# Performance work log

Hardware: AMD Instinct MI355X
Metric: run time of the kernel (lower is better)

Reference implementation:

```python
import jax, jax.numpy as jnp
import numpy as np

NUM_LEVELS = 6
LEVEL_DIM = 4
BASE_RES = 4
HASHMAP_SIZE = 2 ** 19  # torch-ngp default log2_hashmap_size=19
N_SAMPLES = 300
PRIMES = (1, 2654435761, 805459861)
N_RAYS = 16384

# offsets of the 8 trilinear corners, [8,3]
_OFFS = jnp.array([[i, j, k] for i in (0, 1) for j in (0, 1) for k in (0, 1)], dtype=jnp.int32)


def _sample_points_along_ray(starts, ends):
    # starts/ends: [N,2]; lerp 300 points, append ray parameter t as z -> [N,300,3]
    t = jnp.linspace(0.0, 1.0, N_SAMPLES, dtype=starts.dtype)[None, :, None]  # [1,300,1]
    p2 = starts[:, None, :] * (1.0 - t) + ends[:, None, :] * t  # [N,300,2]
    z = jnp.broadcast_to(t, (starts.shape[0], N_SAMPLES, 1))
    return jnp.concatenate([p2, z], axis=-1)


def _grid_encode(points, embeddings):
    # points: [N,S,3] in [0,1]; embeddings: [L, T, D]. Returns [N,S,L*D].
    feats = []
    for l in range(NUM_LEVELS):
        R = BASE_RES * (2 ** l)  # 4,8,16,32,64,128
        pos = points * R
        p0 = jnp.floor(pos).astype(jnp.int32)
        w = pos - p0  # trilinear fractions, [N,S,3]
        corners = jnp.clip(p0[..., None, :] + _OFFS, 0, R)  # [N,S,8,3]
        cw = jnp.where(_OFFS.astype(bool), w[..., None, :], 1.0 - w[..., None, :]).prod(-1)  # [N,S,8]
        if (R + 1) ** 3 <= HASHMAP_SIZE:
            # dense level: row-major vertex index
            idx = corners[..., 0] + corners[..., 1] * (R + 1) + corners[..., 2] * (R + 1) ** 2
        else:
            # hashed level: xor of coord * prime, uint32 wraparound
            c = corners.astype(jnp.uint32)
            idx = ((c[..., 0] * jnp.uint32(PRIMES[0]))
                   ^ (c[..., 1] * jnp.uint32(PRIMES[1]))
                   ^ (c[..., 2] * jnp.uint32(PRIMES[2]))) % jnp.uint32(HASHMAP_SIZE)
            idx = idx.astype(jnp.int32)
        emb = embeddings[l][idx]  # [N,S,8,D] gather
        feats.append((cw[..., None] * emb).sum(-2))  # [N,S,D]
    return jnp.concatenate(feats, axis=-1)  # [N,S,24]


def setup_inputs() -> dict:
    key = jax.random.key(0)
    ks = jax.random.split(key, 12)
    x = jax.random.uniform(ks[0], (N_RAYS, 4), dtype=jnp.float32)
    indices_first = jax.random.randint(ks[1], (N_RAYS,), 0, N_SAMPLES, dtype=jnp.int32)
    # hash-grid tables, torch-ngp init: uniform(-1e-4, 1e-4)
    embeddings = jax.random.uniform(ks[2], (NUM_LEVELS, HASHMAP_SIZE, LEVEL_DIM),
                                    minval=-1e-4, maxval=1e-4, dtype=jnp.float32)
    d_in = NUM_LEVELS * LEVEL_DIM * 5  # 120
    sc = 0.02
    W1 = jax.random.normal(ks[3], (64, d_in), dtype=jnp.float32) * sc
    b1 = jnp.zeros((64,), jnp.float32)
    W2 = jax.random.normal(ks[4], (64, 64), dtype=jnp.float32) * sc
    b2 = jnp.zeros((64,), jnp.float32)
    W3 = jax.random.normal(ks[5], (64, 64), dtype=jnp.float32) * sc
    b3 = jnp.zeros((64,), jnp.float32)
    W4 = jax.random.normal(ks[6], (3, 64), dtype=jnp.float32) * sc
    b4 = jnp.zeros((3,), jnp.float32)
    return {"x": x, "indices_first": indices_first, "embeddings": embeddings,
            "W1": W1, "b1": b1, "W2": W2, "b2": b2, "W3": W3, "b3": b3, "W4": W4, "b4": b4}


def reference(x, indices_first, embeddings, W1, b1, W2, b2, W3, b3, W4, b4):
    pts = jax.lax.stop_gradient(_sample_points_along_ray(x[:, :2], x[:, 2:4]))  # no_grad in original
    pe = _grid_encode(pts, embeddings)  # [N,300,24]
    n = jnp.arange(x.shape[0])
    gather = lambda d: pe[n, jnp.clip(indices_first + d, 0, N_SAMPLES - 1)]
    feat = jnp.concatenate([gather(-2), gather(-1), gather(0), gather(1), gather(2)], axis=-1)  # [N,120]
    h = jax.nn.relu(feat @ W1.T + b1)
    h = jax.nn.relu(h @ W2.T + b2)
    h = jax.nn.relu(h @ W3.T + b3)
    return h @ W4.T + b4  # [N,3]
```

## Files before the change

### kernel.cpp

```cpp
#include <hip/hip_runtime.h>


#define NSAMP 300
#define HSIZE (1u << 19)

__global__ __launch_bounds__(1024, 1) void rgbnet_fused(
    const float4* __restrict__ x,
    const int*    __restrict__ idxf,
    const float4* __restrict__ emb,
    const float* __restrict__ W1, const float* __restrict__ b1,
    const float* __restrict__ W2, const float* __restrict__ b2,
    const float* __restrict__ W3, const float* __restrict__ b3,
    const float* __restrict__ W4, const float* __restrict__ b4,
    float* __restrict__ out, int N)
{
    __shared__ float sFeat[120 * 64];
    __shared__ float sHa[64 * 64];
    __shared__ float sHb[64 * 64];

    const int tid  = threadIdx.x;
    const int r    = tid & 63;
    const int wsub = tid >> 6;
    const int ray  = blockIdx.x * 64 + r;

    {
        const float4 xr = x[ray];
        const int    i0 = idxf[ray];
        const float sx = xr.x, sy = xr.y, ex = xr.z, ey = xr.w;

        for (int p = wsub; p < 30; p += 16) {
            const int d = p / 6;
            const int l = p - d * 6;
            int s = i0 + d - 2;
            s = max(0, min(s, NSAMP - 1));
            const float t   = (float)s * (1.0f / 299.0f);
            const float omt = 1.0f - t;
            const int   R   = 4 << l;
            const float fR  = (float)R;
            const float px = (sx * omt + ex * t) * fR;
            const float py = (sy * omt + ey * t) * fR;
            const float pz = t * fR;
            const float fx0 = floorf(px), fy0 = floorf(py), fz0 = floorf(pz);
            const float wx = px - fx0, wy = py - fy0, wz = pz - fz0;
            const int ix = (int)fx0, iy = (int)fy0, iz = (int)fz0;
            const int Rp1 = R + 1;
            const float4* __restrict__ ebase = emb + (size_t)l * HSIZE;

            float ax = 0.f, ay = 0.f, az = 0.f, aw = 0.f;
            #pragma unroll
            for (int c = 0; c < 8; ++c) {
                const int ox = (c >> 2) & 1, oy = (c >> 1) & 1, oz = c & 1;
                int cx = min(ix + ox, R); cx = max(cx, 0);
                int cy = min(iy + oy, R); cy = max(cy, 0);
                int cz = min(iz + oz, R); cz = max(cz, 0);
                unsigned idx;
                if (l < 5) {
                    idx = (unsigned)(cx + cy * Rp1 + cz * Rp1 * Rp1);
                } else {
                    idx = ((unsigned)cx * 1u
                         ^ (unsigned)cy * 2654435761u
                         ^ (unsigned)cz * 805459861u) & (HSIZE - 1u);
                }
                const float4 e = ebase[idx];
                const float cw = (ox ? wx : 1.f - wx)
                               * (oy ? wy : 1.f - wy)
                               * (oz ? wz : 1.f - wz);
                ax = fmaf(cw, e.x, ax);
                ay = fmaf(cw, e.y, ay);
                az = fmaf(cw, e.z, az);
                aw = fmaf(cw, e.w, aw);
            }
            const int k0 = p * 4;
            sFeat[(k0 + 0) * 64 + r] = ax;
            sFeat[(k0 + 1) * 64 + r] = ay;
            sFeat[(k0 + 2) * 64 + r] = az;
            sFeat[(k0 + 3) * 64 + r] = aw;
        }
    }
    __syncthreads();

    const int wu = __builtin_amdgcn_readfirstlane(wsub);
    const int j0 = wu * 4;

    float hh[4];

    #pragma unroll
    for (int jj = 0; jj < 4; ++jj) hh[jj] = b1[j0 + jj];
    #pragma unroll 2
    for (int kc = 0; kc < 120; kc += 4) {
        const float f0 = sFeat[(kc + 0) * 64 + r];
        const float f1 = sFeat[(kc + 1) * 64 + r];
        const float f2 = sFeat[(kc + 2) * 64 + r];
        const float f3 = sFeat[(kc + 3) * 64 + r];
        #pragma unroll
        for (int jj = 0; jj < 4; ++jj) {
            const float4 wv = *(const float4*)&W1[(j0 + jj) * 120 + kc];
            hh[jj] = fmaf(f0, wv.x, hh[jj]);
            hh[jj] = fmaf(f1, wv.y, hh[jj]);
            hh[jj] = fmaf(f2, wv.z, hh[jj]);
            hh[jj] = fmaf(f3, wv.w, hh[jj]);
        }
    }
    #pragma unroll
    for (int jj = 0; jj < 4; ++jj)
        sHa[(j0 + jj) * 64 + r] = fmaxf(hh[jj], 0.f);
    __syncthreads();

    #pragma unroll
    for (int jj = 0; jj < 4; ++jj) hh[jj] = b2[j0 + jj];
    #pragma unroll 2
    for (int kc = 0; kc < 64; kc += 4) {
        const float f0 = sHa[(kc + 0) * 64 + r];
        const float f1 = sHa[(kc + 1) * 64 + r];
        const float f2 = sHa[(kc + 2) * 64 + r];
        const float f3 = sHa[(kc + 3) * 64 + r];
        #pragma unroll
        for (int jj = 0; jj < 4; ++jj) {
            const float4 wv = *(const float4*)&W2[(j0 + jj) * 64 + kc];
            hh[jj] = fmaf(f0, wv.x, hh[jj]);
            hh[jj] = fmaf(f1, wv.y, hh[jj]);
            hh[jj] = fmaf(f2, wv.z, hh[jj]);
            hh[jj] = fmaf(f3, wv.w, hh[jj]);
        }
    }
    #pragma unroll
    for (int jj = 0; jj < 4; ++jj)
        sHb[(j0 + jj) * 64 + r] = fmaxf(hh[jj], 0.f);
    __syncthreads();

    #pragma unroll
    for (int jj = 0; jj < 4; ++jj) hh[jj] = b3[j0 + jj];
    #pragma unroll 2
    for (int kc = 0; kc < 64; kc += 4) {
        const float f0 = sHb[(kc + 0) * 64 + r];
        const float f1 = sHb[(kc + 1) * 64 + r];
        const float f2 = sHb[(kc + 2) * 64 + r];
        const float f3 = sHb[(kc + 3) * 64 + r];
        #pragma unroll
        for (int jj = 0; jj < 4; ++jj) {
            const float4 wv = *(const float4*)&W3[(j0 + jj) * 64 + kc];
            hh[jj] = fmaf(f0, wv.x, hh[jj]);
            hh[jj] = fmaf(f1, wv.y, hh[jj]);
            hh[jj] = fmaf(f2, wv.z, hh[jj]);
            hh[jj] = fmaf(f3, wv.w, hh[jj]);
        }
    }
    #pragma unroll
    for (int jj = 0; jj < 4; ++jj)
        sHa[(j0 + jj) * 64 + r] = fmaxf(hh[jj], 0.f);
    __syncthreads();

    if (wu < 3) {
        float acc = b4[wu];
        #pragma unroll 2
        for (int kc = 0; kc < 64; kc += 4) {
            const float f0 = sHa[(kc + 0) * 64 + r];
            const float f1 = sHa[(kc + 1) * 64 + r];
            const float f2 = sHa[(kc + 2) * 64 + r];
            const float f3 = sHa[(kc + 3) * 64 + r];
            const float4 wv = *(const float4*)&W4[wu * 64 + kc];
            acc = fmaf(f0, wv.x, acc);
            acc = fmaf(f1, wv.y, acc);
            acc = fmaf(f2, wv.z, acc);
            acc = fmaf(f3, wv.w, acc);
        }
        out[(size_t)ray * 3 + wu] = acc;
    }
}

extern "C" void kernel_launch(void* const* d_in, const int* in_sizes, int n_in,
                              void* d_out, int out_size, void* d_ws, size_t ws_size,
                              hipStream_t stream) {
    const float4* x    = (const float4*)d_in[0];
    const int*    idxf = (const int*)   d_in[1];
    const float4* emb  = (const float4*)d_in[2];
    const float*  W1   = (const float*) d_in[3];
    const float*  b1   = (const float*) d_in[4];
    const float*  W2   = (const float*) d_in[5];
    const float*  b2   = (const float*) d_in[6];
    const float*  W3   = (const float*) d_in[7];
    const float*  b3   = (const float*) d_in[8];
    const float*  W4   = (const float*) d_in[9];
    const float*  b4   = (const float*) d_in[10];
    float* out = (float*)d_out;

    const int N = in_sizes[0] / 4;
    const int blocks = (N + 63) / 64;
    hipLaunchKernelGGL(rgbnet_fused, dim3(blocks), dim3(1024), 0, stream,
                       x, idxf, emb, W1, b1, W2, b2, W3, b3, W4, b4, out, N);
}
```

Measured before the change: 130.6 us.

## Split fused kernel into separate encode and MLP kernels via workspace

Splits the fused grid-encode plus MLP kernel into two launches. A 256-thread encode kernel with a 2D grid handles one (ray, level, offset) pair per thread and writes features to global workspace. A separate MLP kernel reads them into shared memory in a ray-major padded layout with float4 LDS reads, and reuses shared buffers so several blocks can fit per CU. The aim is better occupancy and latency hiding for the random embedding gathers, plus cheaper LDS access, at the cost of a global round trip for the features and an extra launch.

```diff
diff --git a/kernel.cpp b/kernel.cpp
--- a/kernel.cpp
+++ b/kernel.cpp
@@ -4,167 +4,176 @@
 #define NSAMP 300
 #define HSIZE (1u << 19)
 
-__global__ __launch_bounds__(1024, 1) void rgbnet_fused(
+__global__ __launch_bounds__(256, 6) void encode_kernel(
     const float4* __restrict__ x,
     const int*    __restrict__ idxf,
     const float4* __restrict__ emb,
+    float4*       __restrict__ feat,
+    int N)
+{
+    const int tid = threadIdx.x;
+    const int r   = tid & 63;
+    const int p   = blockIdx.y * 4 + (tid >> 6);
+    const int ray = blockIdx.x * 64 + r;
+    if (p >= 30) return;
+
+    const float4 xr = x[ray];
+    const int    i0 = idxf[ray];
+    const int d = p / 6;
+    const int l = p - d * 6;
+    int s = i0 + d - 2;
+    s = max(0, min(s, NSAMP - 1));
+    const float t   = (float)s * (1.0f / 299.0f);
+    const float omt = 1.0f - t;
+    const int   R   = 4 << l;
+    const float fR  = (float)R;
+    const float px = (xr.x * omt + xr.z * t) * fR;
+    const float py = (xr.y * omt + xr.w * t) * fR;
+    const float pz = t * fR;
+    const float fx0 = floorf(px), fy0 = floorf(py), fz0 = floorf(pz);
+    const float wx = px - fx0, wy = py - fy0, wz = pz - fz0;
+    const int ix = (int)fx0, iy = (int)fy0, iz = (int)fz0;
+    const int Rp1 = R + 1;
+    const float4* __restrict__ ebase = emb + (size_t)l * HSIZE;
+
+    float ax = 0.f, ay = 0.f, az = 0.f, aw = 0.f;
+    #pragma unroll
+    for (int c = 0; c < 8; ++c) {
+        const int ox = (c >> 2) & 1, oy = (c >> 1) & 1, oz = c & 1;
+        int cx = min(ix + ox, R); cx = max(cx, 0);
+        int cy = min(iy + oy, R); cy = max(cy, 0);
+        int cz = min(iz + oz, R); cz = max(cz, 0);
+        unsigned idx;
+        if (l < 5) {
+            idx = (unsigned)(cx + cy * Rp1 + cz * Rp1 * Rp1);
+        } else {
+            idx = ((unsigned)cx * 1u
+                 ^ (unsigned)cy * 2654435761u
+                 ^ (unsigned)cz * 805459861u) & (HSIZE - 1u);
+        }
+        const float4 e = ebase[idx];
+        const float cw = (ox ? wx : 1.f - wx)
+                       * (oy ? wy : 1.f - wy)
+                       * (oz ? wz : 1.f - wz);
+        ax = fmaf(cw, e.x, ax);
+        ay = fmaf(cw, e.y, ay);
+        az = fmaf(cw, e.z, az);
+        aw = fmaf(cw, e.w, aw);
+    }
+    feat[(size_t)p * N + ray] = make_float4(ax, ay, az, aw);
+}
+
+__global__ __launch_bounds__(1024, 4) void mlp_kernel(
+    const float4* __restrict__ feat,
     const float* __restrict__ W1, const float* __restrict__ b1,
     const float* __restrict__ W2, const float* __restrict__ b2,
     const float* __restrict__ W3, const float* __restrict__ b3,
     const float* __restrict__ W4, const float* __restrict__ b4,
     float* __restrict__ out, int N)
 {
-    __shared__ float sFeat[120 * 64];
-    __shared__ float sHa[64 * 64];
-    __shared__ float sHb[64 * 64];
-
-    const int tid  = threadIdx.x;
-    const int r    = tid & 63;
-    const int wsub = tid >> 6;
-    const int ray  = blockIdx.x * 64 + r;
-
-    {
-        const float4 xr = x[ray];
-        const int    i0 = idxf[ray];
-        const float sx = xr.x, sy = xr.y, ex = xr.z, ey = xr.w;
-
-        for (int p = wsub; p < 30; p += 16) {
-            const int d = p / 6;
-            const int l = p - d * 6;
-            int s = i0 + d - 2;
-            s = max(0, min(s, NSAMP - 1));
-            const float t   = (float)s * (1.0f / 299.0f);
-            const float omt = 1.0f - t;
-            const int   R   = 4 << l;
-            const float fR  = (float)R;
-            const float px = (sx * omt + ex * t) * fR;
-            const float py = (sy * omt + ey * t) * fR;
-            const float pz = t * fR;
-            const float fx0 = floorf(px), fy0 = floorf(py), fz0 = floorf(pz);
-            const float wx = px - fx0, wy = py - fy0, wz = pz - fz0;
-            const int ix = (int)fx0, iy = (int)fy0, iz = (int)fz0;
-            const int Rp1 = R + 1;
-            const float4* __restrict__ ebase = emb + (size_t)l * HSIZE;
-
-            float ax = 0.f, ay = 0.f, az = 0.f, aw = 0.f;
-            #pragma unroll
-            for (int c = 0; c < 8; ++c) {
-                const int ox = (c >> 2) & 1, oy = (c >> 1) & 1, oz = c & 1;
-                int cx = min(ix + ox, R); cx = max(cx, 0);
-                int cy = min(iy + oy, R); cy = max(cy, 0);
-                int cz = min(iz + oz, R); cz = max(cz, 0);
-                unsigned idx;
-                if (l < 5) {
-                    idx = (unsigned)(cx + cy * Rp1 + cz * Rp1 * Rp1);
-                } else {
-                    idx = ((unsigned)cx * 1u
-                         ^ (unsigned)cy * 2654435761u
-                         ^ (unsigned)cz * 805459861u) & (HSIZE - 1u);
-                }
-                const float4 e = ebase[idx];
-                const float cw = (ox ? wx : 1.f - wx)
-                               * (oy ? wy : 1.f - wy)
-                               * (oz ? wz : 1.f - wz);
-                ax = fmaf(cw, e.x, ax);
-                ay = fmaf(cw, e.y, ay);
-                az = fmaf(cw, e.z, az);
-                aw = fmaf(cw, e.w, aw);
-            }
-            const int k0 = p * 4;
-            sFeat[(k0 + 0) * 64 + r] = ax;
-            sFeat[(k0 + 1) * 64 + r] = ay;
-            sFeat[(k0 + 2) * 64 + r] = az;
-            sFeat[(k0 + 3) * 64 + r] = aw;
-        }
-    }
-    __syncthreads();
-
-    const int wu = __builtin_amdgcn_readfirstlane(wsub);
-    const int j0 = wu * 4;
-
+    __shared__ float sm[12288];
+    float* sFeat = sm;
+    float* sHa   = sm + 7936;
+    float* sHb   = sm;
+
+    const int tid = threadIdx.x;
+    const int r   = tid & 63;
+    const int w   = tid >> 6;
+    const int ray = blockIdx.x * 64 + r;
+
+    {
+        const float4 v = feat[(size_t)w * N + ray];
+        *(float4*)&sFeat[r * 124 + w * 4] = v;
+        if (w < 14) {
+            const float4 v2 = feat[(size_t)(w + 16) * N + ray];
+            *(float4*)&sFeat[r * 124 + (w + 16) * 4] = v2;
+        }
+    }
+    __syncthreads();
+
+    const int j0 = w * 4;
     float hh[4];
 
     #pragma unroll
     for (int jj = 0; jj < 4; ++jj) hh[jj] = b1[j0 + jj];
     #pragma unroll 2
     for (int kc = 0; kc < 120; kc += 4) {
-        const float f0 = sFeat[(kc + 0) * 64 + r];
-        const float f1 = sFeat[(kc + 1) * 64 + r];
-        const float f2 = sFeat[(kc + 2) * 64 + r];
-        const float f3 = sFeat[(kc + 3) * 64 + r];
+        const float4 f = *(const float4*)&sFeat[r * 124 + kc];
         #pragma unroll
         for (int jj = 0; jj < 4; ++jj) {
             const float4 wv = *(const float4*)&W1[(j0 + jj) * 120 + kc];
-            hh[jj] = fmaf(f0, wv.x, hh[jj]);
-            hh[jj] = fmaf(f1, wv.y, hh[jj]);
-            hh[jj] = fmaf(f2, wv.z, hh[jj]);
-            hh[jj] = fmaf(f3, wv.w, hh[jj]);
-        }
-    }
-    #pragma unroll
-    for (int jj = 0; jj < 4; ++jj)
-        sHa[(j0 + jj) * 64 + r] = fmaxf(hh[jj], 0.f);
+            hh[jj] = fmaf(f.x, wv.x, hh[jj]);
+            hh[jj] = fmaf(f.y, wv.y, hh[jj]);
+            hh[jj] = fmaf(f.z, wv.z, hh[jj]);
+            hh[jj] = fmaf(f.w, wv.w, hh[jj]);
+        }
+    }
+    {
+        float4 o;
+        o.x = fmaxf(hh[0], 0.f); o.y = fmaxf(hh[1], 0.f);
+        o.z = fmaxf(hh[2], 0.f); o.w = fmaxf(hh[3], 0.f);
+        *(float4*)&sHa[r * 68 + j0] = o;
+    }
     __syncthreads();
 
     #pragma unroll
     for (int jj = 0; jj < 4; ++jj) hh[jj] = b2[j0 + jj];
     #pragma unroll 2
     for (int kc = 0; kc < 64; kc += 4) {
-        const float f0 = sHa[(kc + 0) * 64 + r];
-        const float f1 = sHa[(kc + 1) * 64 + r];
-        const float f2 = sHa[(kc + 2) * 64 + r];
-        const float f3 = sHa[(kc + 3) * 64 + r];
+        const float4 f = *(const float4*)&sHa[r * 68 + kc];
         #pragma unroll
         for (int jj = 0; jj < 4; ++jj) {
             const float4 wv = *(const float4*)&W2[(j0 + jj) * 64 + kc];
-            hh[jj] = fmaf(f0, wv.x, hh[jj]);
-            hh[jj] = fmaf(f1, wv.y, hh[jj]);
-            hh[jj] = fmaf(f2, wv.z, hh[jj]);
-            hh[jj] = fmaf(f3, wv.w, hh[jj]);
-        }
-    }
-    #pragma unroll
-    for (int jj = 0; jj < 4; ++jj)
-        sHb[(j0 + jj) * 64 + r] = fmaxf(hh[jj], 0.f);
+            hh[jj] = fmaf(f.x, wv.x, hh[jj]);
+            hh[jj] = fmaf(f.y, wv.y, hh[jj]);
+            hh[jj] = fmaf(f.z, wv.z, hh[jj]);
+            hh[jj] = fmaf(f.w, wv.w, hh[jj]);
+        }
+    }
+    __syncthreads();
+    {
+        float4 o;
+        o.x = fmaxf(hh[0], 0.f); o.y = fmaxf(hh[1], 0.f);
+        o.z = fmaxf(hh[2], 0.f); o.w = fmaxf(hh[3], 0.f);
+        *(float4*)&sHb[r * 68 + j0] = o;
+    }
     __syncthreads();
 
     #pragma unroll
     for (int jj = 0; jj < 4; ++jj) hh[jj] = b3[j0 + jj];
     #pragma unroll 2
     for (int kc = 0; kc < 64; kc += 4) {
-        const float f0 = sHb[(kc + 0) * 64 + r];
-        const float f1 = sHb[(kc + 1) * 64 + r];
-        const float f2 = sHb[(kc + 2) * 64 + r];
-        const float f3 = sHb[(kc + 3) * 64 + r];
+        const float4 f = *(const float4*)&sHb[r * 68 + kc];
         #pragma unroll
         for (int jj = 0; jj < 4; ++jj) {
             const float4 wv = *(const float4*)&W3[(j0 + jj) * 64 + kc];
-            hh[jj] = fmaf(f0, wv.x, hh[jj]);
-            hh[jj] = fmaf(f1, wv.y, hh[jj]);
-            hh[jj] = fmaf(f2, wv.z, hh[jj]);
-            hh[jj] = fmaf(f3, wv.w, hh[jj]);
-        }
-    }
-    #pragma unroll
-    for (int jj = 0; jj < 4; ++jj)
-        sHa[(j0 + jj) * 64 + r] = fmaxf(hh[jj], 0.f);
-    __syncthreads();
-
-    if (wu < 3) {
-        float acc = b4[wu];
+            hh[jj] = fmaf(f.x, wv.x, hh[jj]);
+            hh[jj] = fmaf(f.y, wv.y, hh[jj]);
+            hh[jj] = fmaf(f.z, wv.z, hh[jj]);
+            hh[jj] = fmaf(f.w, wv.w, hh[jj]);
+        }
+    }
+    __syncthreads();
+    {
+        float4 o;
+        o.x = fmaxf(hh[0], 0.f); o.y = fmaxf(hh[1], 0.f);
+        o.z = fmaxf(hh[2], 0.f); o.w = fmaxf(hh[3], 0.f);
+        *(float4*)&sHa[r * 68 + j0] = o;
+    }
+    __syncthreads();
+
+    if (w < 3) {
+        float acc = b4[w];
         #pragma unroll 2
         for (int kc = 0; kc < 64; kc += 4) {
-            const float f0 = sHa[(kc + 0) * 64 + r];
-            const float f1 = sHa[(kc + 1) * 64 + r];
-            const float f2 = sHa[(kc + 2) * 64 + r];
-            const float f3 = sHa[(kc + 3) * 64 + r];
-            const float4 wv = *(const float4*)&W4[wu * 64 + kc];
-            acc = fmaf(f0, wv.x, acc);
-            acc = fmaf(f1, wv.y, acc);
-            acc = fmaf(f2, wv.z, acc);
-            acc = fmaf(f3, wv.w, acc);
-        }
-        out[(size_t)ray * 3 + wu] = acc;
+            const float4 f  = *(const float4*)&sHa[r * 68 + kc];
+            const float4 wv = *(const float4*)&W4[w * 64 + kc];
+            acc = fmaf(f.x, wv.x, acc);
+            acc = fmaf(f.y, wv.y, acc);
+            acc = fmaf(f.z, wv.z, acc);
+            acc = fmaf(f.w, wv.w, acc);
+        }
+        out[(size_t)ray * 3 + w] = acc;
     }
 }
 
@@ -185,7 +194,11 @@
     float* out = (float*)d_out;
 
     const int N = in_sizes[0] / 4;
-    const int blocks = (N + 63) / 64;
-    hipLaunchKernelGGL(rgbnet_fused, dim3(blocks), dim3(1024), 0, stream,
-                       x, idxf, emb, W1, b1, W2, b2, W3, b3, W4, b4, out, N);
+    float4* feat = (float4*)d_ws;
+
+    const int rayblocks = (N + 63) / 64;
+    hipLaunchKernelGGL(encode_kernel, dim3(rayblocks, 8), dim3(256), 0, stream,
+                       x, idxf, emb, feat, N);
+    hipLaunchKernelGGL(mlp_kernel, dim3(rayblocks), dim3(1024), 0, stream,
+                       feat, W1, b1, W2, b2, W3, b3, W4, b4, out, N);
 }
```

New measurement: 146.2 us. +12.0%, slower.

## Shrink blocks to 32 rays with 512 threads, split waves across units

Applied to the files above, without the earlier changes.

Each block now handles 32 rays with 512 threads. Each 64-lane wave is split into two half-waves, and each half-wave is one of 16 work units covering the same layout as before. Shared memory is cut by aliasing the layer-2 output buffer onto the feature buffer, and launch bounds now ask for 6 blocks per CU, aiming for higher occupancy and better latency hiding on the random embedding gathers. The cost is that within a wave the two halves read different weight rows, which may lose the uniform, scalar-friendly weight loads the old code had through readfirstlane.

```diff
diff --git a/kernel.cpp b/kernel.cpp
--- a/kernel.cpp
+++ b/kernel.cpp
@@ -3,8 +3,9 @@
 
 #define NSAMP 300
 #define HSIZE (1u << 19)
+#define RAYS 32
 
-__global__ __launch_bounds__(1024, 1) void rgbnet_fused(
+__global__ __launch_bounds__(512, 6) void rgbnet_fused(
     const float4* __restrict__ x,
     const int*    __restrict__ idxf,
     const float4* __restrict__ emb,
@@ -14,21 +15,24 @@
     const float* __restrict__ W4, const float* __restrict__ b4,
     float* __restrict__ out, int N)
 {
-    __shared__ float sFeat[120 * 64];
-    __shared__ float sHa[64 * 64];
-    __shared__ float sHb[64 * 64];
+    __shared__ float sm[120 * RAYS + 64 * RAYS];
+    float* sFeat = sm;
+    float* sHa   = sm + 120 * RAYS;
+    float* sHb   = sm;
 
     const int tid  = threadIdx.x;
-    const int r    = tid & 63;
-    const int wsub = tid >> 6;
-    const int ray  = blockIdx.x * 64 + r;
+    const int lane = tid & 63;
+    const int r    = lane & 31;
+    const int half = lane >> 5;
+    const int w    = tid >> 6;
+    const int u    = w * 2 + half;
+    const int ray  = blockIdx.x * RAYS + r;
 
     {
         const float4 xr = x[ray];
         const int    i0 = idxf[ray];
-        const float sx = xr.x, sy = xr.y, ex = xr.z, ey = xr.w;
 
-        for (int p = wsub; p < 30; p += 16) {
+        for (int p = u; p < 30; p += 16) {
             const int d = p / 6;
             const int l = p - d * 6;
             int s = i0 + d - 2;
@@ -37,8 +41,8 @@
             const float omt = 1.0f - t;
             const int   R   = 4 << l;
             const float fR  = (float)R;
-            const float px = (sx * omt + ex * t) * fR;
-            const float py = (sy * omt + ey * t) * fR;
+            const float px = (xr.x * omt + xr.z * t) * fR;
+            const float py = (xr.y * omt + xr.w * t) * fR;
             const float pz = t * fR;
             const float fx0 = floorf(px), fy0 = floorf(py), fz0 = floorf(pz);
             const float wx = px - fx0, wy = py - fy0, wz = pz - fz0;
@@ -71,27 +75,27 @@
                 aw = fmaf(cw, e.w, aw);
             }
             const int k0 = p * 4;
-            sFeat[(k0 + 0) * 64 + r] = ax;
-            sFeat[(k0 + 1) * 64 + r] = ay;
-            sFeat[(k0 + 2) * 64 + r] = az;
-            sFeat[(k0 + 3) * 64 + r] = aw;
+            sFeat[(k0 + 0) * RAYS + r] = ax;
+            sFeat[(k0 + 1) * RAYS + r] = ay;
+            sFeat[(k0 + 2) * RAYS + r] = az;
+            sFeat[(k0 + 3) * RAYS + r] = aw;
         }
     }
     __syncthreads();
 
-    const int wu = __builtin_amdgcn_readfirstlane(wsub);
-    const int j0 = wu * 4;
-
+    const int j0 = w * 8 + half * 4;
     float hh[4];
 
-    #pragma unroll
-    for (int jj = 0; jj < 4; ++jj) hh[jj] = b1[j0 + jj];
+    {
+        const float4 bv = *(const float4*)&b1[j0];
+        hh[0] = bv.x; hh[1] = bv.y; hh[2] = bv.z; hh[3] = bv.w;
+    }
     #pragma unroll 2
     for (int kc = 0; kc < 120; kc += 4) {
-        const float f0 = sFeat[(kc + 0) * 64 + r];
-        const float f1 = sFeat[(kc + 1) * 64 + r];
-        const float f2 = sFeat[(kc + 2) * 64 + r];
-        const float f3 = sFeat[(kc + 3) * 64 + r];
+        const float f0 = sFeat[(kc + 0) * RAYS + r];
+        const float f1 = sFeat[(kc + 1) * RAYS + r];
+        const float f2 = sFeat[(kc + 2) * RAYS + r];
+        const float f3 = sFeat[(kc + 3) * RAYS + r];
         #pragma unroll
         for (int jj = 0; jj < 4; ++jj) {
             const float4 wv = *(const float4*)&W1[(j0 + jj) * 120 + kc];
@@ -103,17 +107,19 @@
     }
     #pragma unroll
     for (int jj = 0; jj < 4; ++jj)
-        sHa[(j0 + jj) * 64 + r] = fmaxf(hh[jj], 0.f);
+        sHa[(j0 + jj) * RAYS + r] = fmaxf(hh[jj], 0.f);
     __syncthreads();
 
-    #pragma unroll
-    for (int jj = 0; jj < 4; ++jj) hh[jj] = b2[j0 + jj];
+    {
+        const float4 bv = *(const float4*)&b2[j0];
+        hh[0] = bv.x; hh[1] = bv.y; hh[2] = bv.z; hh[3] = bv.w;
+    }
     #pragma unroll 2
     for (int kc = 0; kc < 64; kc += 4) {
-        const float f0 = sHa[(kc + 0) * 64 + r];
-        const float f1 = sHa[(kc + 1) * 64 + r];
-        const float f2 = sHa[(kc + 2) * 64 + r];
-        const float f3 = sHa[(kc + 3) * 64 + r];
+        const float f0 = sHa[(kc + 0) * RAYS + r];
+        const float f1 = sHa[(kc + 1) * RAYS + r];
+        const float f2 = sHa[(kc + 2) * RAYS + r];
+        const float f3 = sHa[(kc + 3) * RAYS + r];
         #pragma unroll
         for (int jj = 0; jj < 4; ++jj) {
             const float4 wv = *(const float4*)&W2[(j0 + jj) * 64 + kc];
@@ -125,17 +131,19 @@
     }
     #pragma unroll
     for (int jj = 0; jj < 4; ++jj)
-        sHb[(j0 + jj) * 64 + r] = fmaxf(hh[jj], 0.f);
+        sHb[(j0 + jj) * RAYS + r] = fmaxf(hh[jj], 0.f);
     __syncthreads();
 
-    #pragma unroll
-    for (int jj = 0; jj < 4; ++jj) hh[jj] = b3[j0 + jj];
+    {
+        const float4 bv = *(const float4*)&b3[j0];
+        hh[0] = bv.x; hh[1] = bv.y; hh[2] = bv.z; hh[3] = bv.w;
+    }
     #pragma unroll 2
     for (int kc = 0; kc < 64; kc += 4) {
-        const float f0 = sHb[(kc + 0) * 64 + r];
-        const float f1 = sHb[(kc + 1) * 64 + r];
-        const float f2 = sHb[(kc + 2) * 64 + r];
-        const float f3 = sHb[(kc + 3) * 64 + r];
+        const float f0 = sHb[(kc + 0) * RAYS + r];
+        const float f1 = sHb[(kc + 1) * RAYS + r];
+        const float f2 = sHb[(kc + 2) * RAYS + r];
+        const float f3 = sHb[(kc + 3) * RAYS + r];
         #pragma unroll
         for (int jj = 0; jj < 4; ++jj) {
             const float4 wv = *(const float4*)&W3[(j0 + jj) * 64 + kc];
@@ -147,24 +155,24 @@
     }
     #pragma unroll
     for (int jj = 0; jj < 4; ++jj)
-        sHa[(j0 + jj) * 64 + r] = fmaxf(hh[jj], 0.f);
+        sHa[(j0 + jj) * RAYS + r] = fmaxf(hh[jj], 0.f);
     __syncthreads();
 
-    if (wu < 3) {
-        float acc = b4[wu];
+    if (u < 3) {
+        float acc = b4[u];
         #pragma unroll 2
         for (int kc = 0; kc < 64; kc += 4) {
-            const float f0 = sHa[(kc + 0) * 64 + r];
-            const float f1 = sHa[(kc + 1) * 64 + r];
-            const float f2 = sHa[(kc + 2) * 64 + r];
-            const float f3 = sHa[(kc + 3) * 64 + r];
-            const float4 wv = *(const float4*)&W4[wu * 64 + kc];
+            const float f0 = sHa[(kc + 0) * RAYS + r];
+            const float f1 = sHa[(kc + 1) * RAYS + r];
+            const float f2 = sHa[(kc + 2) * RAYS + r];
+            const float f3 = sHa[(kc + 3) * RAYS + r];
+            const float4 wv = *(const float4*)&W4[u * 64 + kc];
             acc = fmaf(f0, wv.x, acc);
             acc = fmaf(f1, wv.y, acc);
             acc = fmaf(f2, wv.z, acc);
             acc = fmaf(f3, wv.w, acc);
         }
-        out[(size_t)ray * 3 + wu] = acc;
+        out[(size_t)ray * 3 + u] = acc;
     }
 }
 
@@ -185,7 +193,7 @@
     float* out = (float*)d_out;
 
     const int N = in_sizes[0] / 4;
-    const int blocks = (N + 63) / 64;
-    hipLaunchKernelGGL(rgbnet_fused, dim3(blocks), dim3(1024), 0, stream,
+    const int blocks = (N + RAYS - 1) / RAYS;
+    hipLaunchKernelGGL(rgbnet_fused, dim3(blocks), dim3(512), 0, stream,
                        x, idxf, emb, W1, b1, W2, b2, W3, b3, W4, b4, out, N);
 }
```

Result: slower. 140.8 us (+7.8%).
